# Optimization experiments

Measured on AMD Instinct MI355X. Metric: run time of the kernel, lower is better.

The kernel has to match this reference:

```python
import jax, jax.numpy as jnp
import numpy as np

NUM_CLASSES = 16
ABSENT_SCORE = 1.0  # score for classes absent in both pred and target


def setup_inputs() -> dict:
    key = jax.random.key(0)
    k1, k2 = jax.random.split(key)
    pred = jax.random.normal(k1, (8, NUM_CLASSES, 512, 512), dtype=jnp.float32)
    target = jax.random.randint(k2, (8, 512, 512), 0, NUM_CLASSES, dtype=jnp.int32)
    return {"pred": pred, "target": target}


def reference(pred, target):
    # argmax over class channel -> hard labels (B,H,W), then flatten
    p = jnp.argmax(pred, axis=1).reshape(-1).astype(jnp.int32)
    t = target.reshape(-1).astype(jnp.int32)
    # single-pass histogram replacing the per-class loop:
    # intersection[c] = #{i : p[i]==c and t[i]==c} = bincount of p restricted to p==t
    counts_p = jnp.bincount(p, length=NUM_CLASSES)
    counts_t = jnp.bincount(t, length=NUM_CLASSES)
    inter = jnp.bincount(p, weights=(p == t).astype(jnp.float32), length=NUM_CLASSES)
    union = counts_p.astype(jnp.float32) + counts_t.astype(jnp.float32) - inter
    scores = jnp.where(union == 0, jnp.float32(ABSENT_SCORE), inter / jnp.where(union == 0, 1.0, union))
    return scores.mean()  # reduction='mean'
```

## Files before the change

kernel.cpp:

```cpp
#include <hip/hip_runtime.h>
#include <stdint.h>

#define NUM_CLASSES 16
#define HW (512 * 512)
#define NPIX (8 * HW)
#define NVEC (NPIX / 4)
#define HBLOCKS 2048
#define PAD 32
#define GHIST_DWORDS (256 * PAD)

__global__ __launch_bounds__(256) void jaccard_hist_kernel(
    const float* __restrict__ pred,
    const int* __restrict__ target,
    unsigned int* __restrict__ ghist) {
  __shared__ unsigned int lh[256];
  lh[threadIdx.x] = 0u;
  __syncthreads();

  int tid = blockIdx.x * 256 + threadIdx.x;
  int idx4 = tid << 2;
  int b = idx4 >> 18;
  int hw = idx4 & (HW - 1);
  const float* base = pred + (size_t)b * (NUM_CLASSES * HW) + hw;

  float4 best = *(const float4*)(base);
  int ax = 0, ay = 0, az = 0, aw = 0;
#pragma unroll
  for (int c = 1; c < NUM_CLASSES; ++c) {
    float4 v = *(const float4*)(base + (size_t)c * HW);
    if (v.x > best.x) { best.x = v.x; ax = c; }
    if (v.y > best.y) { best.y = v.y; ay = c; }
    if (v.z > best.z) { best.z = v.z; az = c; }
    if (v.w > best.w) { best.w = v.w; aw = c; }
  }

  int4 t = *(const int4*)(target + idx4);
  atomicAdd(&lh[(ax << 4) + t.x], 1u);
  atomicAdd(&lh[(ay << 4) + t.y], 1u);
  atomicAdd(&lh[(az << 4) + t.z], 1u);
  atomicAdd(&lh[(aw << 4) + t.w], 1u);

  __syncthreads();
  unsigned int v = lh[threadIdx.x];
  if (v) atomicAdd(&ghist[(unsigned)threadIdx.x * PAD], v);
}

__global__ __launch_bounds__(64) void jaccard_finalize_kernel(
    const unsigned int* __restrict__ ghist, float* __restrict__ out) {
  __shared__ unsigned int h[256];
  int l = threadIdx.x;
#pragma unroll
  for (int k = 0; k < 4; ++k) h[l + 64 * k] = ghist[(unsigned)(l + 64 * k) * PAD];
  __syncthreads();

  float score = 0.0f;
  if (l < NUM_CLASSES) {
    unsigned int cp = 0, ct = 0;
#pragma unroll
    for (int j = 0; j < NUM_CLASSES; ++j) {
      cp += h[l * 16 + j];
      ct += h[j * 16 + l];
    }
    unsigned int inter = h[l * 17];
    float uni = (float)cp + (float)ct - (float)inter;
    score = (uni == 0.0f) ? 1.0f : ((float)inter / uni);
  }

#pragma unroll
  for (int off = 8; off >= 1; off >>= 1) score += __shfl_down(score, off, 64);

  if (l == 0) out[0] = score * (1.0f / (float)NUM_CLASSES);
}

extern "C" void kernel_launch(void* const* d_in, const int* in_sizes, int n_in,
                              void* d_out, int out_size, void* d_ws, size_t ws_size,
                              hipStream_t stream) {
  const float* pred = (const float*)d_in[0];
  const int* target = (const int*)d_in[1];
  float* out = (float*)d_out;
  unsigned int* ghist = (unsigned int*)d_ws;

  hipMemsetAsync(d_ws, 0, GHIST_DWORDS * sizeof(unsigned int), stream);

  jaccard_hist_kernel<<<HBLOCKS, 256, 0, stream>>>(pred, target, ghist);
  jaccard_finalize_kernel<<<1, 64, 0, stream>>>(ghist, out);
}
```

Before: 199.1 us.

## Replace global atomic histogram with per-block partials and drop memset

Each histogram block now handles two vector chunks (grid halved) and writes its 256-bin local histogram to a per-block partials buffer instead of issuing global atomics. A 1024-thread finalize kernel reduces all partials before computing the Jaccard scores, and the workspace memset launch is removed. This targets global atomic contention and the extra memset launch, at the cost of a 1 MB partials write/read and a serial single-block reduction.

```diff
diff --git a/kernel.cpp b/kernel.cpp
--- a/kernel.cpp
+++ b/kernel.cpp
@@ -3,73 +3,87 @@
 
 #define NUM_CLASSES 16
 #define HW (512 * 512)
-#define NPIX (8 * HW)
-#define NVEC (NPIX / 4)
-#define HBLOCKS 2048
-#define PAD 32
-#define GHIST_DWORDS (256 * PAD)
+#define NVEC (8 * HW / 4)
+#define HALF (NVEC / 2)
+#define HBLOCKS 1024
 
 __global__ __launch_bounds__(256) void jaccard_hist_kernel(
     const float* __restrict__ pred,
     const int* __restrict__ target,
-    unsigned int* __restrict__ ghist) {
+    unsigned int* __restrict__ parts) {
   __shared__ unsigned int lh[256];
   lh[threadIdx.x] = 0u;
   __syncthreads();
 
   int tid = blockIdx.x * 256 + threadIdx.x;
-  int idx4 = tid << 2;
-  int b = idx4 >> 18;
-  int hw = idx4 & (HW - 1);
-  const float* base = pred + (size_t)b * (NUM_CLASSES * HW) + hw;
 
-  float4 best = *(const float4*)(base);
-  int ax = 0, ay = 0, az = 0, aw = 0;
 #pragma unroll
-  for (int c = 1; c < NUM_CLASSES; ++c) {
-    float4 v = *(const float4*)(base + (size_t)c * HW);
-    if (v.x > best.x) { best.x = v.x; ax = c; }
-    if (v.y > best.y) { best.y = v.y; ay = c; }
-    if (v.z > best.z) { best.z = v.z; az = c; }
-    if (v.w > best.w) { best.w = v.w; aw = c; }
+  for (int half = 0; half < 2; ++half) {
+    int i = tid + half * HALF;
+    int idx4 = i << 2;
+    int b = idx4 >> 18;
+    int hw = idx4 & (HW - 1);
+    const float* base = pred + (size_t)b * (NUM_CLASSES * HW) + hw;
+
+    float4 best = *(const float4*)(base);
+    int ax = 0, ay = 0, az = 0, aw = 0;
+#pragma unroll
+    for (int c = 1; c < NUM_CLASSES; ++c) {
+      float4 v = *(const float4*)(base + (size_t)c * HW);
+      if (v.x > best.x) { best.x = v.x; ax = c; }
+      if (v.y > best.y) { best.y = v.y; ay = c; }
+      if (v.z > best.z) { best.z = v.z; az = c; }
+      if (v.w > best.w) { best.w = v.w; aw = c; }
+    }
+
+    int4 t = *(const int4*)(target + idx4);
+    atomicAdd(&lh[(ax << 4) + t.x], 1u);
+    atomicAdd(&lh[(ay << 4) + t.y], 1u);
+    atomicAdd(&lh[(az << 4) + t.z], 1u);
+    atomicAdd(&lh[(aw << 4) + t.w], 1u);
   }
 
-  int4 t = *(const int4*)(target + idx4);
-  atomicAdd(&lh[(ax << 4) + t.x], 1u);
-  atomicAdd(&lh[(ay << 4) + t.y], 1u);
-  atomicAdd(&lh[(az << 4) + t.z], 1u);
-  atomicAdd(&lh[(aw << 4) + t.w], 1u);
-
   __syncthreads();
-  unsigned int v = lh[threadIdx.x];
-  if (v) atomicAdd(&ghist[(unsigned)threadIdx.x * PAD], v);
+  parts[blockIdx.x * 256 + threadIdx.x] = lh[threadIdx.x];
 }
 
-__global__ __launch_bounds__(64) void jaccard_finalize_kernel(
-    const unsigned int* __restrict__ ghist, float* __restrict__ out) {
+__global__ __launch_bounds__(1024) void jaccard_finalize_kernel(
+    const unsigned int* __restrict__ parts, float* __restrict__ out) {
+  __shared__ unsigned int acc[4][256];
   __shared__ unsigned int h[256];
-  int l = threadIdx.x;
-#pragma unroll
-  for (int k = 0; k < 4; ++k) h[l + 64 * k] = ghist[(unsigned)(l + 64 * k) * PAD];
+  int t = threadIdx.x & 255;
+  int g = threadIdx.x >> 8;
+
+  unsigned int s = 0;
+#pragma unroll 8
+  for (int r = g; r < HBLOCKS; r += 4)
+    s += parts[r * 256 + t];
+  acc[g][t] = s;
   __syncthreads();
 
-  float score = 0.0f;
-  if (l < NUM_CLASSES) {
-    unsigned int cp = 0, ct = 0;
+  if (threadIdx.x < 256)
+    h[threadIdx.x] = acc[0][threadIdx.x] + acc[1][threadIdx.x] +
+                     acc[2][threadIdx.x] + acc[3][threadIdx.x];
+  __syncthreads();
+
+  if (threadIdx.x < 64) {
+    int l = threadIdx.x;
+    float score = 0.0f;
+    if (l < NUM_CLASSES) {
+      unsigned int cp = 0, ct = 0;
 #pragma unroll
-    for (int j = 0; j < NUM_CLASSES; ++j) {
-      cp += h[l * 16 + j];
-      ct += h[j * 16 + l];
+      for (int j = 0; j < NUM_CLASSES; ++j) {
+        cp += h[l * 16 + j];
+        ct += h[j * 16 + l];
+      }
+      unsigned int inter = h[l * 17];
+      float uni = (float)cp + (float)ct - (float)inter;
+      score = (uni == 0.0f) ? 1.0f : ((float)inter / uni);
     }
-    unsigned int inter = h[l * 17];
-    float uni = (float)cp + (float)ct - (float)inter;
-    score = (uni == 0.0f) ? 1.0f : ((float)inter / uni);
+#pragma unroll
+    for (int off = 8; off >= 1; off >>= 1) score += __shfl_down(score, off, 64);
+    if (l == 0) out[0] = score * (1.0f / (float)NUM_CLASSES);
   }
-
-#pragma unroll
-  for (int off = 8; off >= 1; off >>= 1) score += __shfl_down(score, off, 64);
-
-  if (l == 0) out[0] = score * (1.0f / (float)NUM_CLASSES);
 }
 
 extern "C" void kernel_launch(void* const* d_in, const int* in_sizes, int n_in,
@@ -78,10 +92,8 @@
   const float* pred = (const float*)d_in[0];
   const int* target = (const int*)d_in[1];
   float* out = (float*)d_out;
-  unsigned int* ghist = (unsigned int*)d_ws;
+  unsigned int* parts = (unsigned int*)d_ws;
 
-  hipMemsetAsync(d_ws, 0, GHIST_DWORDS * sizeof(unsigned int), stream);
-
-  jaccard_hist_kernel<<<HBLOCKS, 256, 0, stream>>>(pred, target, ghist);
-  jaccard_finalize_kernel<<<1, 64, 0, stream>>>(ghist, out);
+  jaccard_hist_kernel<<<HBLOCKS, 256, 0, stream>>>(pred, target, parts);
+  jaccard_finalize_kernel<<<1, 1024, 0, stream>>>(parts, out);
 }
```

Result: no change. 201.4 us (+1.1%).
